# Optimization experiments

Measured on AMD Instinct MI355X. Metric: run time of the kernel, lower is better.

Reference implementation:

```python
import jax, jax.numpy as jnp
import numpy as np

B, S, H = 1, 2048, 1024
NH, NKV, HD = 16, 4, 64  # n_attn_heads, n_kv_heads, head_dim


def setup_inputs() -> dict:
    key = jax.random.key(0)
    k1, k2, k3, k4 = jax.random.split(key, 4)
    x = jax.random.normal(k1, (B, S, H), dtype=jnp.float32)
    Wq = jax.random.normal(k2, (H, H), dtype=jnp.float32) * 0.02
    Wk = jax.random.normal(k3, (NKV * HD, H), dtype=jnp.float32) * 0.02
    Wv = jax.random.normal(k4, (NKV * HD, H), dtype=jnp.float32) * 0.02
    return {"x": x, "Wq": Wq, "Wk": Wk, "Wv": Wv}


def reference(x, Wq, Wk, Wv):
    b, s, h = x.shape
    rep = NH // NKV
    # projections (torch Linear: x @ W.T)
    q = (x @ Wq.T).reshape(b, s, NH, HD).transpose(0, 2, 1, 3)      # [b, NH, s, d]
    k = (x @ Wk.T).reshape(b, s, NKV, HD).transpose(0, 2, 1, 3)     # [b, NKV, s, d]
    v = (x @ Wv.T).reshape(b, s, NKV, HD).transpose(0, 2, 1, 3)
    # repeat_kv: expand each kv head rep times
    k = jnp.repeat(k, rep, axis=1)                                   # [b, NH, s, d]
    v = jnp.repeat(v, rep, axis=1)
    # NOTE: source scales by 1/sqrt(hidden_size), not 1/sqrt(head_dim)
    scale = 1.0 / np.sqrt(H).astype(np.float32)
    scores = jnp.einsum('bhqd,bhkd->bhqk', q, k) * scale             # [b, NH, s, s]
    causal = jnp.tril(jnp.ones((s, s), dtype=bool))
    scores = jnp.where(causal[None, None], scores, -jnp.inf)
    probs = jax.nn.softmax(scores, axis=-1)
    y = jnp.einsum('bhqk,bhkd->bhqd', probs, v)                      # [b, NH, s, d]
    return y.transpose(0, 2, 1, 3).reshape(b, s, NH * HD)
```

## Files before the change

### kernel.cpp

```cpp
#include <hip/hip_runtime.h>

#define S_LEN 2048
#define HID   1024
#define NHEAD 16
#define NKVH  4
#define HDIM  64
#define NPROJ 1536
#define QKSTR 1280

typedef __bf16 bf16x8 __attribute__((ext_vector_type(8)));
typedef float  f32x4  __attribute__((ext_vector_type(4)));

typedef const __attribute__((address_space(1))) void* gas_ptr;
typedef __attribute__((address_space(3))) void*       las_ptr;

#define QSCALE 0.04508422f

__device__ __forceinline__ unsigned short f2bf(float f) {
    unsigned u = __builtin_bit_cast(unsigned, f);
    u = u + 0x7FFFu + ((u >> 16) & 1u);
    return (unsigned short)(u >> 16);
}

__global__ __launch_bounds__(256) void cvt_all(
    const float* __restrict__ x,  const float* __restrict__ wq,
    const float* __restrict__ wk, const float* __restrict__ wv,
    unsigned short* __restrict__ xbf, unsigned short* __restrict__ wbf)
{
    const long nx  = (long)S_LEN * HID;
    const long nwq = (long)HID * HID;
    const long nwk = (long)256 * HID;
    long i = (long)(blockIdx.x * 256 + threadIdx.x) * 4;
    const float* src; unsigned short* dst;
    if (i < nx)                  { src = x  + i;                 dst = xbf + i; }
    else if (i < nx + nwq)       { long j = i - nx;              src = wq + j; dst = wbf + j; }
    else if (i < nx + nwq + nwk) { long j = i - nx - nwq;        src = wk + j; dst = wbf + nwq + j; }
    else                         { long j = i - nx - nwq - nwk;  src = wv + j; dst = wbf + nwq + nwk + j; }
    float4 v = *(const float4*)src;
    ushort4 o; o.x = f2bf(v.x); o.y = f2bf(v.y); o.z = f2bf(v.z); o.w = f2bf(v.w);
    *(ushort4*)dst = o;
}

__global__ __launch_bounds__(256) void proj_gemm(
    const unsigned short* __restrict__ xbf,
    const unsigned short* __restrict__ wbf,
    unsigned short* __restrict__ qkv,
    unsigned short* __restrict__ vT)
{
    __shared__ unsigned short At[128 * 32];
    __shared__ unsigned short Bt[128 * 32];
    const int tid = threadIdx.x;
    const int w = tid >> 6, l = tid & 63;
    const int quad = l >> 4, lane16 = l & 15;
    const int m0 = blockIdx.y * 128, n0 = blockIdx.x * 128;
    const int wm = (w & 1) * 64, wn = (w >> 1) * 64;

    f32x4 acc[4][4] = {};

    for (int kt = 0; kt < HID; kt += 32) {
        __syncthreads();
        #pragma unroll
        for (int c = 0; c < 2; ++c) {
            const int rbase = c * 64 + w * 16;
            const unsigned short* ga = xbf + (long)(m0 + rbase + (l >> 2)) * HID + kt + (l & 3) * 8;
            __builtin_amdgcn_global_load_lds((gas_ptr)ga, (las_ptr)&At[rbase * 32], 16, 0, 0);
            const unsigned short* gb = wbf + (long)(n0 + rbase + (l >> 2)) * HID + kt + (l & 3) * 8;
            __builtin_amdgcn_global_load_lds((gas_ptr)gb, (las_ptr)&Bt[rbase * 32], 16, 0, 0);
        }
        __syncthreads();

        bf16x8 a[4], b[4];
        #pragma unroll
        for (int mi = 0; mi < 4; ++mi)
            a[mi] = *(const bf16x8*)&At[(wm + mi * 16 + lane16) * 32 + quad * 8];
        #pragma unroll
        for (int ni = 0; ni < 4; ++ni)
            b[ni] = *(const bf16x8*)&Bt[(wn + ni * 16 + lane16) * 32 + quad * 8];
        #pragma unroll
        for (int mi = 0; mi < 4; ++mi)
            #pragma unroll
            for (int ni = 0; ni < 4; ++ni)
                acc[mi][ni] = __builtin_amdgcn_mfma_f32_16x16x32_bf16(a[mi], b[ni], acc[mi][ni], 0, 0, 0);
    }

    #pragma unroll
    for (int mi = 0; mi < 4; ++mi) {
        const int row = m0 + wm + mi * 16 + quad * 4;
        #pragma unroll
        for (int ni = 0; ni < 4; ++ni) {
            const int col = n0 + wn + ni * 16 + lane16;
            #pragma unroll
            for (int r = 0; r < 4; ++r) {
                const float v = acc[mi][ni][r];
                if (col < 1024)
                    qkv[(long)(row + r) * QKSTR + col] = f2bf(v * QSCALE);
                else if (col < 1280)
                    qkv[(long)(row + r) * QKSTR + col] = f2bf(v);
                else
                    vT[(long)(col - 1280) * S_LEN + (row + r)] = f2bf(v);
            }
        }
    }
}

#define KSTR 72
__global__ __launch_bounds__(256) void attn(
    const unsigned short* __restrict__ qkv,
    const unsigned short* __restrict__ vT,
    float* __restrict__ out)
{
    __shared__ unsigned short Kt[64 * KSTR];
    __shared__ unsigned short Vt[64 * KSTR];
    __shared__ unsigned short Pb[4 * 16 * KSTR];

    const int tid = threadIdx.x;
    const int w = tid >> 6, l = tid & 63;
    const int quad = l >> 4, lane16 = l & 15;
    const int bx = blockIdx.x, by = blockIdx.y;
    const int qt = (by & 8) ? (31 - bx) : bx;
    const int h  = by;
    const int kh = h >> 2;
    const int qcol = h * 64;
    const int kcol = 1024 + kh * 64;

    const long qrow = (long)(qt * 64 + w * 16 + lane16);
    bf16x8 qa0 = *(const bf16x8*)&qkv[qrow * QKSTR + qcol + quad * 8];
    bf16x8 qa1 = *(const bf16x8*)&qkv[qrow * QKSTR + qcol + 32 + quad * 8];

    f32x4 o[4] = {};
    float rsum[4] = {0.f, 0.f, 0.f, 0.f};

    unsigned short* pw = &Pb[w * 16 * KSTR];

    const int sr = tid >> 2, ss = tid & 3;
    const long vrow = (long)(kh * 64 + sr) * S_LEN;

    bf16x8 kr0, kr1, vr0, vr1;
    {
        const long gk = (long)sr * QKSTR + kcol + ss * 16;
        kr0 = *(const bf16x8*)&qkv[gk];
        kr1 = *(const bf16x8*)&qkv[gk + 8];
        const long gv = vrow + ss * 16;
        vr0 = *(const bf16x8*)&vT[gv];
        vr1 = *(const bf16x8*)&vT[gv + 8];
    }

    for (int kt = 0; kt <= qt; ++kt) {
        __syncthreads();
        *(bf16x8*)&Kt[sr * KSTR + ss * 16]     = kr0;
        *(bf16x8*)&Kt[sr * KSTR + ss * 16 + 8] = kr1;
        *(bf16x8*)&Vt[sr * KSTR + ss * 16]     = vr0;
        *(bf16x8*)&Vt[sr * KSTR + ss * 16 + 8] = vr1;
        if (kt < qt) {
            const long gk = (long)((kt + 1) * 64 + sr) * QKSTR + kcol + ss * 16;
            kr0 = *(const bf16x8*)&qkv[gk];
            kr1 = *(const bf16x8*)&qkv[gk + 8];
            const long gv = vrow + (kt + 1) * 64 + ss * 16;
            vr0 = *(const bf16x8*)&vT[gv];
            vr1 = *(const bf16x8*)&vT[gv + 8];
        }
        __syncthreads();

        f32x4 sacc[4] = {};
        #pragma unroll
        for (int t = 0; t < 4; ++t) {
            bf16x8 kb0 = *(const bf16x8*)&Kt[(t * 16 + lane16) * KSTR + quad * 8];
            bf16x8 kb1 = *(const bf16x8*)&Kt[(t * 16 + lane16) * KSTR + 32 + quad * 8];
            sacc[t] = __builtin_amdgcn_mfma_f32_16x16x32_bf16(qa0, kb0, sacc[t], 0, 0, 0);
            sacc[t] = __builtin_amdgcn_mfma_f32_16x16x32_bf16(qa1, kb1, sacc[t], 0, 0, 0);
        }

        if (kt == qt) {
            #pragma unroll
            for (int t = 0; t < 4; ++t) {
                const int colw = t * 16 + lane16;
                #pragma unroll
                for (int r = 0; r < 4; ++r)
                    if (colw > w * 16 + quad * 4 + r) sacc[t][r] = -3.0e38f;
            }
        }

        #pragma unroll
        for (int t = 0; t < 4; ++t)
            #pragma unroll
            for (int r = 0; r < 4; ++r) {
                const float p = __builtin_amdgcn_exp2f(sacc[t][r]);
                rsum[r] += p;
                const int row = quad * 4 + r;
                const int col = t * 16 + lane16;
                pw[row * KSTR + (col ^ ((row & 12) << 1))] = f2bf(p);
            }

        __syncthreads();

        #pragma unroll
        for (int ks = 0; ks < 2; ++ks) {
            bf16x8 pa = *(const bf16x8*)&pw[lane16 * KSTR + ((ks * 32 + quad * 8) ^ ((lane16 & 12) << 1))];
            #pragma unroll
            for (int t = 0; t < 4; ++t) {
                bf16x8 vb = *(const bf16x8*)&Vt[(t * 16 + lane16) * KSTR + ks * 32 + quad * 8];
                o[t] = __builtin_amdgcn_mfma_f32_16x16x32_bf16(pa, vb, o[t], 0, 0, 0);
            }
        }
    }

    float inv[4];
    #pragma unroll
    for (int r = 0; r < 4; ++r) {
        float v = rsum[r];
        v += __shfl_xor(v, 1);
        v += __shfl_xor(v, 2);
        v += __shfl_xor(v, 4);
        v += __shfl_xor(v, 8);
        inv[r] = 1.0f / v;
    }
    const int orow = qt * 64 + w * 16 + quad * 4;
    #pragma unroll
    for (int t = 0; t < 4; ++t) {
        const int col = h * 64 + t * 16 + lane16;
        #pragma unroll
        for (int r = 0; r < 4; ++r)
            out[(long)(orow + r) * (NHEAD * HDIM) + col] = o[t][r] * inv[r];
    }
}

extern "C" void kernel_launch(void* const* d_in, const int* in_sizes, int n_in,
                              void* d_out, int out_size, void* d_ws, size_t ws_size,
                              hipStream_t stream) {
    const float* x  = (const float*)d_in[0];
    const float* wq = (const float*)d_in[1];
    const float* wk = (const float*)d_in[2];
    const float* wv = (const float*)d_in[3];
    float* out = (float*)d_out;

    unsigned short* xbf = (unsigned short*)d_ws;
    unsigned short* wbf = xbf + (size_t)S_LEN * HID;
    unsigned short* qkv = wbf + (size_t)NPROJ * HID;
    unsigned short* vT  = qkv + (size_t)S_LEN * QKSTR;

    cvt_all<<<dim3(3584), dim3(256), 0, stream>>>(x, wq, wk, wv, xbf, wbf);
    proj_gemm<<<dim3(NPROJ / 128, S_LEN / 128), dim3(256), 0, stream>>>(xbf, wbf, qkv, vT);
    attn<<<dim3(32, 16), dim3(256), 0, stream>>>(qkv, vT, out);
}
```

Measured before the change: 126.0 us.

## Double-buffer projection GEMM and attention K/V tiles, retile GEMM to 128x96

```diff
diff --git a/kernel.cpp b/kernel.cpp
--- a/kernel.cpp
+++ b/kernel.cpp
@@ -47,47 +47,70 @@
     unsigned short* __restrict__ qkv,
     unsigned short* __restrict__ vT)
 {
-    __shared__ unsigned short At[128 * 32];
-    __shared__ unsigned short Bt[128 * 32];
+    __shared__ unsigned short At[2][128 * 64];
+    __shared__ unsigned short Bt[2][96 * 64];
     const int tid = threadIdx.x;
     const int w = tid >> 6, l = tid & 63;
     const int quad = l >> 4, lane16 = l & 15;
-    const int m0 = blockIdx.y * 128, n0 = blockIdx.x * 128;
-    const int wm = (w & 1) * 64, wn = (w >> 1) * 64;
-
-    f32x4 acc[4][4] = {};
-
-    for (int kt = 0; kt < HID; kt += 32) {
+    const int m0 = blockIdx.y * 128, n0 = blockIdx.x * 96;
+    const int wm = (w & 1) * 64, wn = (w >> 1) * 48;
+
+    const int srow = l >> 3;
+    const int scol = ((l & 7) ^ srow) * 8;
+
+    f32x4 acc[4][3] = {};
+
+    #define STAGE(KT, BUF)                                                              \
+        do {                                                                            \
+            _Pragma("unroll")                                                           \
+            for (int c = 0; c < 4; ++c) {                                               \
+                const int rbase = w * 32 + c * 8;                                       \
+                const unsigned short* ga =                                              \
+                    xbf + (long)(m0 + rbase + srow) * HID + (KT) + scol;                \
+                __builtin_amdgcn_global_load_lds((gas_ptr)ga,                           \
+                    (las_ptr)&At[BUF][rbase * 64], 16, 0, 0);                           \
+            }                                                                           \
+            _Pragma("unroll")                                                           \
+            for (int c = 0; c < 3; ++c) {                                               \
+                const int rbase = w * 24 + c * 8;                                       \
+                const unsigned short* gb =                                              \
+                    wbf + (long)(n0 + rbase + srow) * HID + (KT) + scol;                \
+                __builtin_amdgcn_global_load_lds((gas_ptr)gb,                           \
+                    (las_ptr)&Bt[BUF][rbase * 64], 16, 0, 0);                           \
+            }                                                                           \
+        } while (0)
+
+    STAGE(0, 0);
+
+    for (int i = 0; i < 16; ++i) {
+        const int cur = i & 1;
         __syncthreads();
-        #pragma unroll
-        for (int c = 0; c < 2; ++c) {
-            const int rbase = c * 64 + w * 16;
-            const unsigned short* ga = xbf + (long)(m0 + rbase + (l >> 2)) * HID + kt + (l & 3) * 8;
-            __builtin_amdgcn_global_load_lds((gas_ptr)ga, (las_ptr)&At[rbase * 32], 16, 0, 0);
-            const unsigned short* gb = wbf + (long)(n0 + rbase + (l >> 2)) * HID + kt + (l & 3) * 8;
-            __builtin_amdgcn_global_load_lds((gas_ptr)gb, (las_ptr)&Bt[rbase * 32], 16, 0, 0);
-        }
-        __syncthreads();
-
-        bf16x8 a[4], b[4];
-        #pragma unroll
-        for (int mi = 0; mi < 4; ++mi)
-            a[mi] = *(const bf16x8*)&At[(wm + mi * 16 + lane16) * 32 + quad * 8];
-        #pragma unroll
-        for (int ni = 0; ni < 4; ++ni)
-            b[ni] = *(const bf16x8*)&Bt[(wn + ni * 16 + lane16) * 32 + quad * 8];
-        #pragma unroll
-        for (int mi = 0; mi < 4; ++mi)
-            #pragma unroll
-            for (int ni = 0; ni < 4; ++ni)
-                acc[mi][ni] = __builtin_amdgcn_mfma_f32_16x16x32_bf16(a[mi], b[ni], acc[mi][ni], 0, 0, 0);
-    }
+        if (i + 1 < 16) STAGE((i + 1) * 64, cur ^ 1);
+
+        #pragma unroll
+        for (int ks = 0; ks < 2; ++ks) {
+            const int swz = ((ks * 4 + quad) ^ (lane16 & 7)) * 8;
+            bf16x8 a[4], b[3];
+            #pragma unroll
+            for (int mi = 0; mi < 4; ++mi)
+                a[mi] = *(const bf16x8*)&At[cur][(wm + mi * 16 + lane16) * 64 + swz];
+            #pragma unroll
+            for (int ni = 0; ni < 3; ++ni)
+                b[ni] = *(const bf16x8*)&Bt[cur][(wn + ni * 16 + lane16) * 64 + swz];
+            #pragma unroll
+            for (int mi = 0; mi < 4; ++mi)
+                #pragma unroll
+                for (int ni = 0; ni < 3; ++ni)
+                    acc[mi][ni] = __builtin_amdgcn_mfma_f32_16x16x32_bf16(a[mi], b[ni], acc[mi][ni], 0, 0, 0);
+        }
+    }
+    #undef STAGE
 
     #pragma unroll
     for (int mi = 0; mi < 4; ++mi) {
         const int row = m0 + wm + mi * 16 + quad * 4;
         #pragma unroll
-        for (int ni = 0; ni < 4; ++ni) {
+        for (int ni = 0; ni < 3; ++ni) {
             const int col = n0 + wn + ni * 16 + lane16;
             #pragma unroll
             for (int r = 0; r < 4; ++r) {
@@ -109,8 +132,8 @@
     const unsigned short* __restrict__ vT,
     float* __restrict__ out)
 {
-    __shared__ unsigned short Kt[64 * KSTR];
-    __shared__ unsigned short Vt[64 * KSTR];
+    __shared__ unsigned short Kt[2][64 * KSTR];
+    __shared__ unsigned short Vt[2][64 * KSTR];
     __shared__ unsigned short Pb[4 * 16 * KSTR];
 
     const int tid = threadIdx.x;
@@ -146,11 +169,11 @@
     }
 
     for (int kt = 0; kt <= qt; ++kt) {
-        __syncthreads();
-        *(bf16x8*)&Kt[sr * KSTR + ss * 16]     = kr0;
-        *(bf16x8*)&Kt[sr * KSTR + ss * 16 + 8] = kr1;
-        *(bf16x8*)&Vt[sr * KSTR + ss * 16]     = vr0;
-        *(bf16x8*)&Vt[sr * KSTR + ss * 16 + 8] = vr1;
+        const int cur = kt & 1;
+        *(bf16x8*)&Kt[cur][sr * KSTR + ss * 16]     = kr0;
+        *(bf16x8*)&Kt[cur][sr * KSTR + ss * 16 + 8] = kr1;
+        *(bf16x8*)&Vt[cur][sr * KSTR + ss * 16]     = vr0;
+        *(bf16x8*)&Vt[cur][sr * KSTR + ss * 16 + 8] = vr1;
         if (kt < qt) {
             const long gk = (long)((kt + 1) * 64 + sr) * QKSTR + kcol + ss * 16;
             kr0 = *(const bf16x8*)&qkv[gk];
@@ -164,8 +187,8 @@
         f32x4 sacc[4] = {};
         #pragma unroll
         for (int t = 0; t < 4; ++t) {
-            bf16x8 kb0 = *(const bf16x8*)&Kt[(t * 16 + lane16) * KSTR + quad * 8];
-            bf16x8 kb1 = *(const bf16x8*)&Kt[(t * 16 + lane16) * KSTR + 32 + quad * 8];
+            bf16x8 kb0 = *(const bf16x8*)&Kt[cur][(t * 16 + lane16) * KSTR + quad * 8];
+            bf16x8 kb1 = *(const bf16x8*)&Kt[cur][(t * 16 + lane16) * KSTR + 32 + quad * 8];
             sacc[t] = __builtin_amdgcn_mfma_f32_16x16x32_bf16(qa0, kb0, sacc[t], 0, 0, 0);
             sacc[t] = __builtin_amdgcn_mfma_f32_16x16x32_bf16(qa1, kb1, sacc[t], 0, 0, 0);
         }
@@ -198,7 +221,7 @@
             bf16x8 pa = *(const bf16x8*)&pw[lane16 * KSTR + ((ks * 32 + quad * 8) ^ ((lane16 & 12) << 1))];
             #pragma unroll
             for (int t = 0; t < 4; ++t) {
-                bf16x8 vb = *(const bf16x8*)&Vt[(t * 16 + lane16) * KSTR + ks * 32 + quad * 8];
+                bf16x8 vb = *(const bf16x8*)&Vt[cur][(t * 16 + lane16) * KSTR + ks * 32 + quad * 8];
                 o[t] = __builtin_amdgcn_mfma_f32_16x16x32_bf16(pa, vb, o[t], 0, 0, 0);
             }
         }
@@ -239,6 +262,6 @@
     unsigned short* vT  = qkv + (size_t)S_LEN * QKSTR;
 
     cvt_all<<<dim3(3584), dim3(256), 0, stream>>>(x, wq, wk, wv, xbf, wbf);
-    proj_gemm<<<dim3(NPROJ / 128, S_LEN / 128), dim3(256), 0, stream>>>(xbf, wbf, qkv, vT);
+    proj_gemm<<<dim3(16, 16), dim3(256), 0, stream>>>(xbf, wbf, qkv, vT);
     attn<<<dim3(32, 16), dim3(256), 0, stream>>>(qkv, vT, out);
 }
```

New measurement: 124.1 us. Within noise of the previous version (-1.5%).
